# Kernel tuning notes

Measured on AMD Instinct MI355X. Metric: run time of the kernel, lower is better.

The kernel has to match this reference:

```python
import jax, jax.numpy as jnp
import numpy as np

VOCAB = 50000
D = 256          # vector_dim == hidden size
SEQ = 128
BATCH = 4096
NUM_CLASSES = 5


def setup_inputs() -> dict:
    key = jax.random.key(0)
    ks = jax.random.split(key, 8)
    x = jax.random.randint(ks[0], (BATCH, SEQ), 0, VOCAB, dtype=jnp.int64)
    scale = 1.0 / np.sqrt(D)
    emb = jax.random.normal(ks[1], (VOCAB, D), dtype=jnp.float32)
    emb = emb.at[0].set(0.0)  # padding_idx=0 row is zero
    W_ih = jax.random.uniform(ks[2], (D, D), jnp.float32, -scale, scale)
    W_hh = jax.random.uniform(ks[3], (D, D), jnp.float32, -scale, scale)
    b_ih = jax.random.uniform(ks[4], (D,), jnp.float32, -scale, scale)
    b_hh = jax.random.uniform(ks[5], (D,), jnp.float32, -scale, scale)
    W_cls = jax.random.uniform(ks[6], (NUM_CLASSES, D), jnp.float32, -scale, scale)
    b_cls = jax.random.uniform(ks[7], (NUM_CLASSES,), jnp.float32, -scale, scale)
    return {"x": x, "emb": emb, "W_ih": W_ih, "W_hh": W_hh,
            "b_ih": b_ih, "b_hh": b_hh, "W_cls": W_cls, "b_cls": b_cls}


def reference(x, emb, W_ih, W_hh, b_ih, b_hh, W_cls, b_cls):
    # Embedding lookup: [B, S, D]
    xe = emb[x]
    # Precompute input projections for all timesteps in one GEMM.
    x_proj = jnp.einsum("bsd,hd->bsh", xe, W_ih) + b_ih + b_hh  # [B, S, D]

    def step(h, xp_t):
        h = jnp.tanh(xp_t + h @ W_hh.T)
        return h, None

    h0 = jnp.zeros((x.shape[0], W_hh.shape[0]), dtype=xe.dtype)
    # scan over time axis: [S, B, D]
    h_last, _ = jax.lax.scan(step, h0, jnp.swapaxes(x_proj, 0, 1))
    # classifier on last step
    return h_last @ W_cls.T + b_cls  # [B, 5]
```

## Files before the change

### kernel.cpp

```cpp
#include <hip/hip_runtime.h>
#include <math.h>


typedef __attribute__((ext_vector_type(8))) short bf16x8;
typedef __attribute__((ext_vector_type(4))) float f32x4;

#define LDS_STRIDE 264
#define VOCAB 50000

__device__ __align__(256) unsigned short g_P[VOCAB * 256];

static __device__ __forceinline__ float bf2f(unsigned short u) {
    union { unsigned int i; float f; } v; v.i = ((unsigned int)u) << 16; return v.f;
}
static __device__ __forceinline__ unsigned short f2bf(float f) {
    union { float f; unsigned int i; } v; v.f = f;
    unsigned int r = v.i + 0x7FFFu + ((v.i >> 16) & 1u);
    return (unsigned short)(r >> 16);
}
static __device__ __forceinline__ bf16x8 load8_bf(const float* __restrict__ p) {
    float4 a = ((const float4*)p)[0], b = ((const float4*)p)[1];
    bf16x8 r;
    r[0] = (short)f2bf(a.x); r[1] = (short)f2bf(a.y);
    r[2] = (short)f2bf(a.z); r[3] = (short)f2bf(a.w);
    r[4] = (short)f2bf(b.x); r[5] = (short)f2bf(b.y);
    r[6] = (short)f2bf(b.z); r[7] = (short)f2bf(b.w);
    return r;
}
static __device__ __forceinline__ float fast_tanh(float x) {
    x = fminf(8.f, fmaxf(-8.f, x));
    float e = __expf(2.f * x);
    return 1.f - 2.f * __builtin_amdgcn_rcpf(e + 1.f);
}

__global__ __launch_bounds__(256)
void emb_proj_kernel(const float* __restrict__ emb,
                     const float* __restrict__ W_ih,
                     const float* __restrict__ b_ih,
                     const float* __restrict__ b_hh)
{
    __shared__ __align__(16) unsigned short tin [16 * LDS_STRIDE];
    __shared__ __align__(16) unsigned short tout[16 * LDS_STRIDE];
    const int tid  = threadIdx.x;
    const int lane = tid & 63;
    const int wid  = tid >> 6;
    const int n0   = wid * 64;
    const int row  = tid >> 4, seg = tid & 15;

    bf16x8 wf[4][8];
    float  bias[4];
    #pragma unroll
    for (int nt = 0; nt < 4; ++nt) {
        int n = n0 + nt * 16 + (lane & 15);
        bias[nt] = b_ih[n] + b_hh[n];
        #pragma unroll
        for (int kt = 0; kt < 8; ++kt) {
            int k = (lane >> 4) * 8 + kt * 32;
            wf[nt][kt] = load8_bf(W_ih + n * 256 + k);
        }
    }

    for (int tile = blockIdx.x; tile < 3125; tile += gridDim.x) {
        const int v0 = tile * 16;
        {
            const float* src = emb + (size_t)(v0 + row) * 256 + seg * 16;
            bf16x8 lo = load8_bf(src), hi = load8_bf(src + 8);
            *(bf16x8*)(&tin[row * LDS_STRIDE + seg * 16])     = lo;
            *(bf16x8*)(&tin[row * LDS_STRIDE + seg * 16 + 8]) = hi;
        }
        __syncthreads();

        f32x4 acc[4];
        #pragma unroll
        for (int nt = 0; nt < 4; ++nt) acc[nt] = (f32x4){0.f, 0.f, 0.f, 0.f};
        #pragma unroll
        for (int kt = 0; kt < 8; ++kt) {
            bf16x8 a = *(bf16x8*)(&tin[(lane & 15) * LDS_STRIDE + (lane >> 4) * 8 + kt * 32]);
            #pragma unroll
            for (int nt = 0; nt < 4; ++nt)
                acc[nt] = __builtin_amdgcn_mfma_f32_16x16x32_bf16(a, wf[nt][kt], acc[nt], 0, 0, 0);
        }
        #pragma unroll
        for (int nt = 0; nt < 4; ++nt) {
            int n = n0 + nt * 16 + (lane & 15);
            #pragma unroll
            for (int r = 0; r < 4; ++r)
                tout[((lane >> 4) * 4 + r) * LDS_STRIDE + n] = f2bf(acc[nt][r] + bias[nt]);
        }
        __syncthreads();
        {
            uint4 a0 = *(uint4*)(&tout[row * LDS_STRIDE + seg * 16]);
            uint4 a1 = *(uint4*)(&tout[row * LDS_STRIDE + seg * 16 + 8]);
            uint4* dst = (uint4*)(g_P + (size_t)(v0 + row) * 256 + seg * 16);
            dst[0] = a0; dst[1] = a1;
        }
    }
}

__global__ __launch_bounds__(512, 1)
void rnn_kernel(const int* __restrict__ x,
                const float* __restrict__ W_hh,
                const float* __restrict__ W_cls,
                const float* __restrict__ b_cls,
                float* __restrict__ out)
{
    __shared__ __align__(16) unsigned short h_lds [2][16 * LDS_STRIDE];
    __shared__ __align__(16) unsigned short xp_lds[2][16 * LDS_STRIDE];
    __shared__ __align__(16) int tok_lds[16 * 128];
    __shared__ __align__(16) float wcls_lds[5 * 256];
    __shared__ float bcls_lds[5];

    const int tid   = threadIdx.x;
    const int lane  = tid & 63;
    const int wid   = tid >> 6;
    const int b0    = blockIdx.x * 16;
    const int n0    = wid * 32;
    const int grow  = tid >> 5;
    const int gseg  = tid & 31;

    bf16x8 wf[2][8];
    #pragma unroll
    for (int nt = 0; nt < 2; ++nt) {
        int n = n0 + nt * 16 + (lane & 15);
        #pragma unroll
        for (int kt = 0; kt < 8; ++kt) {
            int k = (lane >> 4) * 8 + kt * 32;
            wf[nt][kt] = load8_bf(W_hh + n * 256 + k);
        }
    }

    ((int4*)tok_lds)[tid] = ((const int4*)(x + (size_t)b0 * 128))[tid];
    if (tid < 320) ((float4*)wcls_lds)[tid] = ((const float4*)W_cls)[tid];
    if (tid < 5)   bcls_lds[tid] = b_cls[tid];
    for (int i = tid; i < 16 * LDS_STRIDE / 2; i += 512) ((unsigned int*)h_lds[0])[i] = 0;

    {
        int tok = x[(size_t)(b0 + grow) * 128];
        tok = min(max(tok, 0), VOCAB - 1);
        float4 p = *(const float4*)(g_P + (size_t)tok * 256 + gseg * 8);
        *(float4*)(&xp_lds[0][grow * LDS_STRIDE + gseg * 8]) = p;
    }
    __syncthreads();

    for (int t = 0; t < 128; ++t) {
        const int buf = t & 1;

        float4 p;
        const bool have = (t + 1) < 128;
        if (have) {
            int tok = tok_lds[grow * 128 + t + 1];
            tok = min(max(tok, 0), VOCAB - 1);
            p = *(const float4*)(g_P + (size_t)tok * 256 + gseg * 8);
        }

        f32x4 acc[2];
        acc[0] = (f32x4){0.f, 0.f, 0.f, 0.f};
        acc[1] = (f32x4){0.f, 0.f, 0.f, 0.f};
        #pragma unroll
        for (int kt = 0; kt < 8; ++kt) {
            bf16x8 a = *(bf16x8*)(&h_lds[buf][(lane & 15) * LDS_STRIDE + (lane >> 4) * 8 + kt * 32]);
            acc[0] = __builtin_amdgcn_mfma_f32_16x16x32_bf16(a, wf[0][kt], acc[0], 0, 0, 0);
            acc[1] = __builtin_amdgcn_mfma_f32_16x16x32_bf16(a, wf[1][kt], acc[1], 0, 0, 0);
        }

        #pragma unroll
        for (int nt = 0; nt < 2; ++nt) {
            int col = n0 + nt * 16 + (lane & 15);
            #pragma unroll
            for (int r = 0; r < 4; ++r) {
                int rrow = (lane >> 4) * 4 + r;
                float v = acc[nt][r] + bf2f(xp_lds[buf][rrow * LDS_STRIDE + col]);
                h_lds[buf ^ 1][rrow * LDS_STRIDE + col] = f2bf(fast_tanh(v));
            }
        }
        if (have)
            *(float4*)(&xp_lds[buf ^ 1][grow * LDS_STRIDE + gseg * 8]) = p;
        __syncthreads();
    }

    if (tid < 80) {
        int row = tid / 5, c = tid % 5;
        float acc = bcls_lds[c];
        for (int k = 0; k < 256; ++k)
            acc += bf2f(h_lds[0][row * LDS_STRIDE + k]) * wcls_lds[c * 256 + k];
        out[(size_t)(b0 + row) * 5 + c] = acc;
    }
}

extern "C" void kernel_launch(void* const* d_in, const int* in_sizes, int n_in,
                              void* d_out, int out_size, void* d_ws, size_t ws_size,
                              hipStream_t stream)
{
    const int*   x     = (const int*)d_in[0];
    const float* emb   = (const float*)d_in[1];
    const float* W_ih  = (const float*)d_in[2];
    const float* W_hh  = (const float*)d_in[3];
    const float* b_ih  = (const float*)d_in[4];
    const float* b_hh  = (const float*)d_in[5];
    const float* W_cls = (const float*)d_in[6];
    const float* b_cls = (const float*)d_in[7];
    float*       out   = (float*)d_out;
    (void)d_ws; (void)ws_size;

    emb_proj_kernel<<<512, 256, 0, stream>>>(emb, W_ih, b_ih, b_hh);
    rnn_kernel<<<256, 512, 0, stream>>>(x, W_hh, W_cls, b_cls, out);
}
```

Baseline: 235.9 us.

## Prefetch embedding tiles and deepen token gather pipeline in RNN loop

The projection kernel now register-prefetches the next embedding tile while computing the current one, and the grid grows from 512 to 768 blocks. The RNN kernel prefetches the projected input two steps ahead instead of one. It also loads the xp values before the MFMA chain and unrolls the time loop by two with precomputed LDS pointers. The aim is to hide global-memory gather latency on the serial recurrence, at the cost of more registers held live.

```diff
diff --git a/kernel.cpp b/kernel.cpp
--- a/kernel.cpp
+++ b/kernel.cpp
@@ -1,5 +1,4 @@
 #include <hip/hip_runtime.h>
-#include <math.h>
 
 
 typedef __attribute__((ext_vector_type(8))) short bf16x8;
@@ -7,6 +6,7 @@
 
 #define LDS_STRIDE 264
 #define VOCAB 50000
+#define NBLK_EMB 768
 
 __device__ __align__(256) unsigned short g_P[VOCAB * 256];
 
@@ -18,14 +18,16 @@
     unsigned int r = v.i + 0x7FFFu + ((v.i >> 16) & 1u);
     return (unsigned short)(r >> 16);
 }
-static __device__ __forceinline__ bf16x8 load8_bf(const float* __restrict__ p) {
-    float4 a = ((const float4*)p)[0], b = ((const float4*)p)[1];
+static __device__ __forceinline__ bf16x8 cvt8(float4 a, float4 b) {
     bf16x8 r;
     r[0] = (short)f2bf(a.x); r[1] = (short)f2bf(a.y);
     r[2] = (short)f2bf(a.z); r[3] = (short)f2bf(a.w);
     r[4] = (short)f2bf(b.x); r[5] = (short)f2bf(b.y);
     r[6] = (short)f2bf(b.z); r[7] = (short)f2bf(b.w);
     return r;
+}
+static __device__ __forceinline__ bf16x8 load8_bf(const float* __restrict__ p) {
+    return cvt8(((const float4*)p)[0], ((const float4*)p)[1]);
 }
 static __device__ __forceinline__ float fast_tanh(float x) {
     x = fminf(8.f, fmaxf(-8.f, x));
@@ -54,19 +56,24 @@
         int n = n0 + nt * 16 + (lane & 15);
         bias[nt] = b_ih[n] + b_hh[n];
         #pragma unroll
-        for (int kt = 0; kt < 8; ++kt) {
-            int k = (lane >> 4) * 8 + kt * 32;
-            wf[nt][kt] = load8_bf(W_ih + n * 256 + k);
-        }
-    }
-
-    for (int tile = blockIdx.x; tile < 3125; tile += gridDim.x) {
-        const int v0 = tile * 16;
-        {
-            const float* src = emb + (size_t)(v0 + row) * 256 + seg * 16;
-            bf16x8 lo = load8_bf(src), hi = load8_bf(src + 8);
-            *(bf16x8*)(&tin[row * LDS_STRIDE + seg * 16])     = lo;
-            *(bf16x8*)(&tin[row * LDS_STRIDE + seg * 16 + 8]) = hi;
+        for (int kt = 0; kt < 8; ++kt)
+            wf[nt][kt] = load8_bf(W_ih + n * 256 + (lane >> 4) * 8 + kt * 32);
+    }
+
+    int tile = blockIdx.x;
+    float4 a0, a1, a2, a3;
+    {
+        const float4* s = (const float4*)(emb + ((size_t)tile * 16 + row) * 256 + seg * 16);
+        a0 = s[0]; a1 = s[1]; a2 = s[2]; a3 = s[3];
+    }
+
+    for (; tile < 3125; tile += NBLK_EMB) {
+        *(bf16x8*)(&tin[row * LDS_STRIDE + seg * 16])     = cvt8(a0, a1);
+        *(bf16x8*)(&tin[row * LDS_STRIDE + seg * 16 + 8]) = cvt8(a2, a3);
+        int tn = tile + NBLK_EMB;
+        if (tn < 3125) {
+            const float4* s = (const float4*)(emb + ((size_t)tn * 16 + row) * 256 + seg * 16);
+            a0 = s[0]; a1 = s[1]; a2 = s[2]; a3 = s[3];
         }
         __syncthreads();
 
@@ -89,10 +96,10 @@
         }
         __syncthreads();
         {
-            uint4 a0 = *(uint4*)(&tout[row * LDS_STRIDE + seg * 16]);
-            uint4 a1 = *(uint4*)(&tout[row * LDS_STRIDE + seg * 16 + 8]);
-            uint4* dst = (uint4*)(g_P + (size_t)(v0 + row) * 256 + seg * 16);
-            dst[0] = a0; dst[1] = a1;
+            uint4 o0 = *(uint4*)(&tout[row * LDS_STRIDE + seg * 16]);
+            uint4 o1 = *(uint4*)(&tout[row * LDS_STRIDE + seg * 16 + 8]);
+            uint4* dst = (uint4*)(g_P + ((size_t)tile * 16 + row) * 256 + seg * 16);
+            dst[0] = o0; dst[1] = o1;
         }
     }
 }
@@ -123,10 +130,8 @@
     for (int nt = 0; nt < 2; ++nt) {
         int n = n0 + nt * 16 + (lane & 15);
         #pragma unroll
-        for (int kt = 0; kt < 8; ++kt) {
-            int k = (lane >> 4) * 8 + kt * 32;
-            wf[nt][kt] = load8_bf(W_hh + n * 256 + k);
-        }
+        for (int kt = 0; kt < 8; ++kt)
+            wf[nt][kt] = load8_bf(W_hh + n * 256 + (lane >> 4) * 8 + kt * 32);
     }
 
     ((int4*)tok_lds)[tid] = ((const int4*)(x + (size_t)b0 * 128))[tid];
@@ -134,47 +139,66 @@
     if (tid < 5)   bcls_lds[tid] = b_cls[tid];
     for (int i = tid; i < 16 * LDS_STRIDE / 2; i += 512) ((unsigned int*)h_lds[0])[i] = 0;
 
+    float4 p_cur;
     {
-        int tok = x[(size_t)(b0 + grow) * 128];
-        tok = min(max(tok, 0), VOCAB - 1);
-        float4 p = *(const float4*)(g_P + (size_t)tok * 256 + gseg * 8);
-        *(float4*)(&xp_lds[0][grow * LDS_STRIDE + gseg * 8]) = p;
+        int t0 = x[(size_t)(b0 + grow) * 128 + 0];
+        t0 = min(max(t0, 0), VOCAB - 1);
+        *(float4*)(&xp_lds[0][grow * LDS_STRIDE + gseg * 8]) =
+            *(const float4*)(g_P + (size_t)t0 * 256 + gseg * 8);
+        int t1 = x[(size_t)(b0 + grow) * 128 + 1];
+        t1 = min(max(t1, 0), VOCAB - 1);
+        p_cur = *(const float4*)(g_P + (size_t)t1 * 256 + gseg * 8);
     }
     __syncthreads();
 
-    for (int t = 0; t < 128; ++t) {
-        const int buf = t & 1;
-
-        float4 p;
-        const bool have = (t + 1) < 128;
-        if (have) {
-            int tok = tok_lds[grow * 128 + t + 1];
+    const int colA = (lane & 15) * LDS_STRIDE + (lane >> 4) * 8;
+    const int colC = ((lane >> 4) * 4) * LDS_STRIDE + n0 + (lane & 15);
+    const unsigned short* hA0 = &h_lds[0][colA];
+    const unsigned short* hA1 = &h_lds[1][colA];
+    const unsigned short* xR0 = &xp_lds[0][colC];
+    const unsigned short* xR1 = &xp_lds[1][colC];
+    unsigned short* hW0 = &h_lds[0][colC];
+    unsigned short* hW1 = &h_lds[1][colC];
+    unsigned short* gw0 = &xp_lds[0][grow * LDS_STRIDE + gseg * 8];
+    unsigned short* gw1 = &xp_lds[1][grow * LDS_STRIDE + gseg * 8];
+
+    auto step = [&](const unsigned short* hA, const unsigned short* xR,
+                    unsigned short* hW, unsigned short* gw, int t) {
+        float4 p_nxt;
+        if (t + 2 < 128) {
+            int tok = tok_lds[grow * 128 + t + 2];
             tok = min(max(tok, 0), VOCAB - 1);
-            p = *(const float4*)(g_P + (size_t)tok * 256 + gseg * 8);
-        }
-
-        f32x4 acc[2];
-        acc[0] = (f32x4){0.f, 0.f, 0.f, 0.f};
-        acc[1] = (f32x4){0.f, 0.f, 0.f, 0.f};
+            p_nxt = *(const float4*)(g_P + (size_t)tok * 256 + gseg * 8);
+        }
+        float xp[2][4];
+        #pragma unroll
+        for (int nt = 0; nt < 2; ++nt)
+            #pragma unroll
+            for (int r = 0; r < 4; ++r)
+                xp[nt][r] = bf2f(xR[r * LDS_STRIDE + nt * 16]);
+        f32x4 acc0 = (f32x4){0.f, 0.f, 0.f, 0.f};
+        f32x4 acc1 = (f32x4){0.f, 0.f, 0.f, 0.f};
         #pragma unroll
         for (int kt = 0; kt < 8; ++kt) {
-            bf16x8 a = *(bf16x8*)(&h_lds[buf][(lane & 15) * LDS_STRIDE + (lane >> 4) * 8 + kt * 32]);
-            acc[0] = __builtin_amdgcn_mfma_f32_16x16x32_bf16(a, wf[0][kt], acc[0], 0, 0, 0);
-            acc[1] = __builtin_amdgcn_mfma_f32_16x16x32_bf16(a, wf[1][kt], acc[1], 0, 0, 0);
-        }
-
-        #pragma unroll
-        for (int nt = 0; nt < 2; ++nt) {
-            int col = n0 + nt * 16 + (lane & 15);
-            #pragma unroll
-            for (int r = 0; r < 4; ++r) {
-                int rrow = (lane >> 4) * 4 + r;
-                float v = acc[nt][r] + bf2f(xp_lds[buf][rrow * LDS_STRIDE + col]);
-                h_lds[buf ^ 1][rrow * LDS_STRIDE + col] = f2bf(fast_tanh(v));
-            }
-        }
-        if (have)
-            *(float4*)(&xp_lds[buf ^ 1][grow * LDS_STRIDE + gseg * 8]) = p;
+            bf16x8 a = *(const bf16x8*)(hA + kt * 32);
+            acc0 = __builtin_amdgcn_mfma_f32_16x16x32_bf16(a, wf[0][kt], acc0, 0, 0, 0);
+            acc1 = __builtin_amdgcn_mfma_f32_16x16x32_bf16(a, wf[1][kt], acc1, 0, 0, 0);
+        }
+        #pragma unroll
+        for (int r = 0; r < 4; ++r) {
+            hW[r * LDS_STRIDE]      = f2bf(fast_tanh(acc0[r] + xp[0][r]));
+            hW[r * LDS_STRIDE + 16] = f2bf(fast_tanh(acc1[r] + xp[1][r]));
+        }
+        if (t + 1 < 128)
+            *(float4*)gw = p_cur;
+        p_cur = p_nxt;
+    };
+
+    #pragma unroll 1
+    for (int t2 = 0; t2 < 64; ++t2) {
+        step(hA0, xR0, hW1, gw1, 2 * t2);
+        __syncthreads();
+        step(hA1, xR1, hW0, gw0, 2 * t2 + 1);
         __syncthreads();
     }
 
@@ -202,6 +226,6 @@
     float*       out   = (float*)d_out;
     (void)d_ws; (void)ws_size;
 
-    emb_proj_kernel<<<512, 256, 0, stream>>>(emb, W_ih, b_ih, b_hh);
+    emb_proj_kernel<<<NBLK_EMB, 256, 0, stream>>>(emb, W_ih, b_ih, b_hh);
     rnn_kernel<<<256, 512, 0, stream>>>(x, W_hh, W_cls, b_cls, out);
 }
```

After: 241.0 us. 1.02x slower.
